# Optimization experiments

Hardware: AMD Instinct MI355X
Metric: run time of the kernel (lower is better)

Reference implementation:

```python
import jax, jax.numpy as jnp
import numpy as np
from jax import lax

B, C_IN, C_OUT, K, STYLE_DIM, H, W = 16, 128, 128, 3, 512, 128, 128
EPS = 1e-8


def setup_inputs() -> dict:
    key = jax.random.key(0)
    k1, k2, k3, k4 = jax.random.split(key, 4)
    x = jax.random.normal(k1, (B, C_IN, H, W), dtype=jnp.float32)
    style_vector = jax.random.normal(k2, (B, STYLE_DIM), dtype=jnp.float32)
    # EqualizedLR(nn.Linear(style_dim, in_channels)): weight ~ N(0,1), bias = 0
    proj_w = jax.random.normal(k3, (C_IN, STYLE_DIM), dtype=jnp.float32)
    proj_b = jnp.zeros((C_IN,), dtype=jnp.float32)
    # base conv weight (1, out, in, k, k) ~ N(0,1)
    weight = jax.random.normal(k4, (1, C_OUT, C_IN, K, K), dtype=jnp.float32)
    return {"x": x, "style_vector": style_vector, "proj_w": proj_w,
            "proj_b": proj_b, "weight": weight}


def reference(x, style_vector, proj_w, proj_b, weight):
    b = x.shape[0]
    # EqualizedLR: scale input by gain / sqrt(fan_in), gain=1, fan_in=style_dim
    scale = 1.0 / jnp.sqrt(jnp.float32(STYLE_DIM))
    style = (style_vector * scale) @ proj_w.T + proj_b          # [b, in]
    # modulate: [1,out,in,k,k] * [b,1,in,1,1] -> [b,out,in,k,k]
    w = weight * style[:, None, :, None, None]
    # demodulate
    demod = lax.rsqrt(jnp.sum(w * w, axis=(2, 3, 4)) + EPS)     # [b, out]
    w = w * demod[:, :, None, None, None]
    # grouped conv with groups=b == per-sample conv; vmap over batch
    pad = K // 2
    def conv_one(xi, wi):
        # xi: [in,H,W], wi: [out,in,k,k]
        return lax.conv_general_dilated(
            xi[None], wi, window_strides=(1, 1),
            padding=[(pad, pad), (pad, pad)],
            dimension_numbers=("NCHW", "OIHW", "NCHW"))[0]
    out = jax.vmap(conv_one)(x, w)                               # [b,out,H,W]
    return out
```

## Files before the change

### kernel.cpp

```cpp
#include <hip/hip_runtime.h>
#include <cstdint>

#define B_   16
#define CIN  128
#define COUT 128
#define SD   512
#define H_   128
#define W_   128

typedef __bf16 bf16x8  __attribute__((ext_vector_type(8)));
typedef float  floatx4 __attribute__((ext_vector_type(4)));
typedef float floatx16 __attribute__((ext_vector_type(16)));

__global__ void style_kernel(const float* __restrict__ sv, const float* __restrict__ pw,
                             const float* __restrict__ pb, float* __restrict__ style) {
    int bid = blockIdx.x;
    int b = bid >> 7, c = bid & 127;
    int lane = threadIdx.x;
    const float* svb = sv + b * SD;
    const float* pwc = pw + (size_t)c * SD;
    float s = 0.f;
#pragma unroll
    for (int i = 0; i < SD; i += 64) s += svb[i + lane] * pwc[i + lane];
#pragma unroll
    for (int off = 32; off > 0; off >>= 1) s += __shfl_down(s, off, 64);
    if (lane == 0) style[b * CIN + c] = s * 0.044194173824159216f + pb[c];
}

__global__ void modw_kernel(const float* __restrict__ weight, const float* __restrict__ style,
                            __bf16* __restrict__ wmod) {
    int bid = blockIdx.x;
    int b = bid >> 7, o = bid & 127;
    int c = threadIdx.x;
    float s = style[b * CIN + c];
    const float* wp = weight + ((size_t)o * CIN + c) * 9;
    float v[9];
    float ss = 0.f;
#pragma unroll
    for (int t = 0; t < 9; ++t) { v[t] = wp[t] * s; ss += v[t] * v[t]; }
#pragma unroll
    for (int off = 32; off > 0; off >>= 1) ss += __shfl_down(ss, off, 64);
    __shared__ float sh[2];
    int wid = c >> 6, lane = c & 63;
    if (lane == 0) sh[wid] = ss;
    __syncthreads();
    float d = rsqrtf(sh[0] + sh[1] + 1e-8f);
    int chunk = c >> 4, ci = c & 15;
#pragma unroll
    for (int t = 0; t < 9; ++t) {
        wmod[(((((size_t)b * 9 + t) * 8 + chunk) * 128 + o) * 16 + ci)] = (__bf16)(v[t] * d);
    }
}

__global__ __launch_bounds__(256)
void xpose_kernel(const float* __restrict__ x, __bf16* __restrict__ xT) {
    __shared__ uint32_t T[4 * 4 * 8 * 32];
    int ch = blockIdx.x;
    int hq = blockIdx.y;
    int b  = blockIdx.z;
    int t  = threadIdx.x;
    int cp = t >> 5;
    int wq = t & 31;
    int c0 = ch * 16 + cp * 2;
    const float* pa = x + (((size_t)b * CIN + c0    ) * H_ + hq * 4) * W_ + wq * 4;
    const float* pc = x + (((size_t)b * CIN + c0 + 1) * H_ + hq * 4) * W_ + wq * 4;
#pragma unroll
    for (int hr = 0; hr < 4; ++hr) {
        floatx4 va = *(const floatx4*)(pa + (size_t)hr * W_);
        floatx4 vb = *(const floatx4*)(pc + (size_t)hr * W_);
#pragma unroll
        for (int j = 0; j < 4; ++j) {
            uint32_t lo = (uint32_t)__builtin_bit_cast(unsigned short, (__bf16)va[j]);
            uint32_t hi = (uint32_t)__builtin_bit_cast(unsigned short, (__bf16)vb[j]);
            T[((hr * 4 + j) * 8 + cp) * 32 + wq] = lo | (hi << 16);
        }
    }
    __syncthreads();
    uint32_t* dst = (uint32_t*)xT + ((((size_t)b * 8 + ch) * H_ + hq * 4) * W_) * 8;
#pragma unroll
    for (int it = 0; it < 8; ++it) {
        int o0 = it * 512 + t * 2;
        int cpr = o0 & 7;
        int w   = (o0 >> 3) & 127;
        int hr  = o0 >> 10;
        int base = ((hr * 4 + (w & 3)) * 8);
        uint32_t v0 = T[(base + cpr    ) * 32 + (w >> 2)];
        uint32_t v1 = T[(base + cpr + 1) * 32 + (w >> 2)];
        uint2 pk; pk.x = v0; pk.y = v1;
        *(uint2*)(dst + o0) = pk;
    }
}

#define WXT 66
__global__ __launch_bounds__(256, 2)
void conv_kernel(const __bf16* __restrict__ xT, const __bf16* __restrict__ wmod,
                 float* __restrict__ out) {
    __shared__ __align__(16) __bf16 Xs[2][4 * WXT * 16];
    int w0 = blockIdx.x * 64;
    int h0 = blockIdx.y * 2;
    int b  = blockIdx.z;
    int tid = threadIdx.x;
    int wv = tid >> 6, lane = tid & 63;
    int n = lane & 31, hf = lane >> 5;
    int obase = (wv & 1) * 64;
    int r = wv >> 1;

    floatx16 acc[2][2];
#pragma unroll
    for (int i = 0; i < 2; ++i)
#pragma unroll
        for (int j = 0; j < 2; ++j)
#pragma unroll
            for (int k = 0; k < 16; ++k) acc[i][j][k] = 0.f;

    const __bf16* xb = xT + (size_t)b * 8 * H_ * W_ * 16;

    bool sact[3], sval[3];
    const __bf16* sptr[3];
    int soff[3];
#pragma unroll
    for (int s = 0; s < 3; ++s) {
        int idx = tid + s * 256;
        bool act = (s < 2) || (tid < 16);
        int row = idx / 132;
        int rem = idx - row * 132;
        int wp = rem >> 1, g = rem & 1;
        int hh = h0 - 1 + row, ww = w0 - 1 + wp;
        sact[s] = act;
        sval[s] = act && (unsigned)hh < (unsigned)H_ && (unsigned)ww < (unsigned)W_;
        sptr[s] = xb + ((size_t)hh * W_ + ww) * 16 + g * 8;
        soff[s] = idx * 8;
    }

    bf16x8 sv[3];
#pragma unroll
    for (int s = 0; s < 3; ++s) {
#pragma unroll
        for (int k = 0; k < 8; ++k) sv[s][k] = (__bf16)0.f;
        if (sval[s]) sv[s] = *(const bf16x8*)(sptr[s]);
    }

    const __bf16* apb = wmod + ((((size_t)b * 9) * 8) * 128 + obase + n) * 16 + hf * 8;

    for (int ch = 0; ch < 8; ++ch) {
        bf16x8 a[9][2];
#pragma unroll
        for (int tap = 0; tap < 9; ++tap) {
            const __bf16* ap = apb + tap * 16384 + ch * 2048;
            a[tap][0] = *(const bf16x8*)ap;
            a[tap][1] = *(const bf16x8*)(ap + 512);
        }
        __bf16* xbuf = Xs[ch & 1];
#pragma unroll
        for (int s = 0; s < 3; ++s)
            if (sact[s]) *(bf16x8*)(xbuf + soff[s]) = sv[s];
        if (ch < 7) {
#pragma unroll
            for (int s = 0; s < 3; ++s) {
#pragma unroll
                for (int k = 0; k < 8; ++k) sv[s][k] = (__bf16)0.f;
                if (sval[s]) sv[s] = *(const bf16x8*)(sptr[s] + (size_t)(ch + 1) * (H_ * W_ * 16));
            }
        }
        __syncthreads();
#pragma unroll
        for (int tap = 0; tap < 9; ++tap) {
            int kh = tap / 3, kw = tap % 3;
            int row = r + kh;
#pragma unroll
            for (int wt = 0; wt < 2; ++wt) {
                int wp = wt * 32 + n + kw;
                bf16x8 bfrag = *(const bf16x8*)(xbuf + (row * WXT + wp) * 16 + hf * 8);
                acc[0][wt] = __builtin_amdgcn_mfma_f32_32x32x16_bf16(a[tap][0], bfrag, acc[0][wt], 0, 0, 0);
                acc[1][wt] = __builtin_amdgcn_mfma_f32_32x32x16_bf16(a[tap][1], bfrag, acc[1][wt], 0, 0, 0);
            }
        }
    }

    float* ob = out + (((size_t)b * COUT) * H_ + (h0 + r)) * W_ + w0;
#pragma unroll
    for (int i = 0; i < 2; ++i) {
#pragma unroll
        for (int reg = 0; reg < 16; ++reg) {
            int o = obase + i * 32 + (reg & 3) + 8 * (reg >> 2) + 4 * hf;
#pragma unroll
            for (int wt = 0; wt < 2; ++wt)
                __builtin_nontemporal_store(acc[i][wt][reg],
                    &ob[(size_t)o * (H_ * W_) + wt * 32 + n]);
        }
    }
}

extern "C" void kernel_launch(void* const* d_in, const int* in_sizes, int n_in,
                              void* d_out, int out_size, void* d_ws, size_t ws_size,
                              hipStream_t stream) {
    const float* x      = (const float*)d_in[0];
    const float* sv     = (const float*)d_in[1];
    const float* pw     = (const float*)d_in[2];
    const float* pb     = (const float*)d_in[3];
    const float* weight = (const float*)d_in[4];
    float* out = (float*)d_out;

    float*  style = (float*)d_ws;
    __bf16* wmod  = (__bf16*)((char*)d_ws + 8192);
    __bf16* xT    = (__bf16*)((char*)d_ws + 8192 + 4718592);

    style_kernel<<<B_ * CIN, 64, 0, stream>>>(sv, pw, pb, style);
    modw_kernel<<<B_ * COUT, 128, 0, stream>>>(weight, style, wmod);
    xpose_kernel<<<dim3(8, 32, B_), 256, 0, stream>>>(x, xT);
    conv_kernel<<<dim3(2, 64, B_), 256, 0, stream>>>(xT, wmod, out);
}
```

Measured before the change: 305.4 us.

## Fuse input transpose into conv kernel with swizzled all-channel LDS tile

Removes the separate transpose kernel and its bf16 workspace round-trip. The conv kernel now reads fp32 NCHW input directly, converts it to bf16 and stages all 128 channels of a 4x66 halo tile into XOR-swizzled shared memory in one pass. The per-channel-chunk double buffering and per-chunk syncs are gone. Each wave now computes all 128 output channels for one row and one half-width, with a 3-deep software-pipelined prefetch of weight fragments across the 72 tap/chunk iterations. In exchange, shared memory grows to about 66KB per block, which may limit occupancy, and the input is staged without overlapping its load with compute.

```diff
diff --git a/kernel.cpp b/kernel.cpp
--- a/kernel.cpp
+++ b/kernel.cpp
@@ -52,141 +52,115 @@
     }
 }
 
-__global__ __launch_bounds__(256)
-void xpose_kernel(const float* __restrict__ x, __bf16* __restrict__ xT) {
-    __shared__ uint32_t T[4 * 4 * 8 * 32];
-    int ch = blockIdx.x;
-    int hq = blockIdx.y;
-    int b  = blockIdx.z;
-    int t  = threadIdx.x;
-    int cp = t >> 5;
-    int wq = t & 31;
-    int c0 = ch * 16 + cp * 2;
-    const float* pa = x + (((size_t)b * CIN + c0    ) * H_ + hq * 4) * W_ + wq * 4;
-    const float* pc = x + (((size_t)b * CIN + c0 + 1) * H_ + hq * 4) * W_ + wq * 4;
-#pragma unroll
-    for (int hr = 0; hr < 4; ++hr) {
-        floatx4 va = *(const floatx4*)(pa + (size_t)hr * W_);
-        floatx4 vb = *(const floatx4*)(pc + (size_t)hr * W_);
-#pragma unroll
-        for (int j = 0; j < 4; ++j) {
-            uint32_t lo = (uint32_t)__builtin_bit_cast(unsigned short, (__bf16)va[j]);
-            uint32_t hi = (uint32_t)__builtin_bit_cast(unsigned short, (__bf16)vb[j]);
-            T[((hr * 4 + j) * 8 + cp) * 32 + wq] = lo | (hi << 16);
-        }
-    }
-    __syncthreads();
-    uint32_t* dst = (uint32_t*)xT + ((((size_t)b * 8 + ch) * H_ + hq * 4) * W_) * 8;
-#pragma unroll
-    for (int it = 0; it < 8; ++it) {
-        int o0 = it * 512 + t * 2;
-        int cpr = o0 & 7;
-        int w   = (o0 >> 3) & 127;
-        int hr  = o0 >> 10;
-        int base = ((hr * 4 + (w & 3)) * 8);
-        uint32_t v0 = T[(base + cpr    ) * 32 + (w >> 2)];
-        uint32_t v1 = T[(base + cpr + 1) * 32 + (w >> 2)];
-        uint2 pk; pk.x = v0; pk.y = v1;
-        *(uint2*)(dst + o0) = pk;
-    }
-}
-
-#define WXT 66
 __global__ __launch_bounds__(256, 2)
-void conv_kernel(const __bf16* __restrict__ xT, const __bf16* __restrict__ wmod,
+void conv_kernel(const float* __restrict__ x, const __bf16* __restrict__ wmod,
                  float* __restrict__ out) {
-    __shared__ __align__(16) __bf16 Xs[2][4 * WXT * 16];
+    __shared__ __align__(16) __bf16 Xs[4 * 66 * 128];
     int w0 = blockIdx.x * 64;
     int h0 = blockIdx.y * 2;
     int b  = blockIdx.z;
     int tid = threadIdx.x;
-    int wv = tid >> 6, lane = tid & 63;
-    int n = lane & 31, hf = lane >> 5;
-    int obase = (wv & 1) * 64;
-    int r = wv >> 1;
 
-    floatx16 acc[2][2];
+    {
+        int p = tid >> 2, row = tid & 3;
+        int hh = h0 - 1 + row;
+        bool rowok = (unsigned)hh < (unsigned)H_;
+        const float* b0 = x + (((size_t)b * CIN + 2 * p) * H_ + (rowok ? hh : 0)) * W_;
+        const float* b1 = b0 + H_ * W_;
+        int ch = p >> 3, g = (p >> 2) & 1, ep = (p & 3) * 2;
+        int robase = row * 66;
+        {
+            float v0 = 0.f, v1 = 0.f;
+            if (rowok && w0 > 0) { v0 = b0[w0 - 1]; v1 = b1[w0 - 1]; }
+            uint32_t pk = (uint32_t)__builtin_bit_cast(unsigned short, (__bf16)v0)
+                        | ((uint32_t)__builtin_bit_cast(unsigned short, (__bf16)v1) << 16);
+            int off = robase * 128 + ((ch ^ 0) * 2 + g) * 8 + ep;
+            *(uint32_t*)(Xs + off) = pk;
+        }
+        {
+            float v0 = 0.f, v1 = 0.f;
+            int w = w0 + 64;
+            if (rowok && w < W_) { v0 = b0[w]; v1 = b1[w]; }
+            uint32_t pk = (uint32_t)__builtin_bit_cast(unsigned short, (__bf16)v0)
+                        | ((uint32_t)__builtin_bit_cast(unsigned short, (__bf16)v1) << 16);
+            int off = (robase + 65) * 128 + ((ch ^ (65 & 7)) * 2 + g) * 8 + ep;
+            *(uint32_t*)(Xs + off) = pk;
+        }
 #pragma unroll
-    for (int i = 0; i < 2; ++i)
+        for (int j = 0; j < 16; ++j) {
+            floatx4 va = {0.f, 0.f, 0.f, 0.f}, vb = {0.f, 0.f, 0.f, 0.f};
+            if (rowok) {
+                va = *(const floatx4*)(b0 + w0 + j * 4);
+                vb = *(const floatx4*)(b1 + w0 + j * 4);
+            }
 #pragma unroll
-        for (int j = 0; j < 2; ++j)
-#pragma unroll
-            for (int k = 0; k < 16; ++k) acc[i][j][k] = 0.f;
-
-    const __bf16* xb = xT + (size_t)b * 8 * H_ * W_ * 16;
-
-    bool sact[3], sval[3];
-    const __bf16* sptr[3];
-    int soff[3];
-#pragma unroll
-    for (int s = 0; s < 3; ++s) {
-        int idx = tid + s * 256;
-        bool act = (s < 2) || (tid < 16);
-        int row = idx / 132;
-        int rem = idx - row * 132;
-        int wp = rem >> 1, g = rem & 1;
-        int hh = h0 - 1 + row, ww = w0 - 1 + wp;
-        sact[s] = act;
-        sval[s] = act && (unsigned)hh < (unsigned)H_ && (unsigned)ww < (unsigned)W_;
-        sptr[s] = xb + ((size_t)hh * W_ + ww) * 16 + g * 8;
-        soff[s] = idx * 8;
-    }
-
-    bf16x8 sv[3];
-#pragma unroll
-    for (int s = 0; s < 3; ++s) {
-#pragma unroll
-        for (int k = 0; k < 8; ++k) sv[s][k] = (__bf16)0.f;
-        if (sval[s]) sv[s] = *(const bf16x8*)(sptr[s]);
-    }
-
-    const __bf16* apb = wmod + ((((size_t)b * 9) * 8) * 128 + obase + n) * 16 + hf * 8;
-
-    for (int ch = 0; ch < 8; ++ch) {
-        bf16x8 a[9][2];
-#pragma unroll
-        for (int tap = 0; tap < 9; ++tap) {
-            const __bf16* ap = apb + tap * 16384 + ch * 2048;
-            a[tap][0] = *(const bf16x8*)ap;
-            a[tap][1] = *(const bf16x8*)(ap + 512);
-        }
-        __bf16* xbuf = Xs[ch & 1];
-#pragma unroll
-        for (int s = 0; s < 3; ++s)
-            if (sact[s]) *(bf16x8*)(xbuf + soff[s]) = sv[s];
-        if (ch < 7) {
-#pragma unroll
-            for (int s = 0; s < 3; ++s) {
-#pragma unroll
-                for (int k = 0; k < 8; ++k) sv[s][k] = (__bf16)0.f;
-                if (sval[s]) sv[s] = *(const bf16x8*)(sptr[s] + (size_t)(ch + 1) * (H_ * W_ * 16));
-            }
-        }
-        __syncthreads();
-#pragma unroll
-        for (int tap = 0; tap < 9; ++tap) {
-            int kh = tap / 3, kw = tap % 3;
-            int row = r + kh;
-#pragma unroll
-            for (int wt = 0; wt < 2; ++wt) {
-                int wp = wt * 32 + n + kw;
-                bf16x8 bfrag = *(const bf16x8*)(xbuf + (row * WXT + wp) * 16 + hf * 8);
-                acc[0][wt] = __builtin_amdgcn_mfma_f32_32x32x16_bf16(a[tap][0], bfrag, acc[0][wt], 0, 0, 0);
-                acc[1][wt] = __builtin_amdgcn_mfma_f32_32x32x16_bf16(a[tap][1], bfrag, acc[1][wt], 0, 0, 0);
+            for (int k = 0; k < 4; ++k) {
+                int wp = j * 4 + 1 + k;
+                uint32_t pk = (uint32_t)__builtin_bit_cast(unsigned short, (__bf16)va[k])
+                            | ((uint32_t)__builtin_bit_cast(unsigned short, (__bf16)vb[k]) << 16);
+                int off = (robase + wp) * 128 + ((ch ^ (wp & 7)) * 2 + g) * 8 + ep;
+                *(uint32_t*)(Xs + off) = pk;
             }
         }
     }
+    __syncthreads();
 
-    float* ob = out + (((size_t)b * COUT) * H_ + (h0 + r)) * W_ + w0;
+    int wv = tid >> 6, lane = tid & 63;
+    int n = lane & 31, hf = lane >> 5;
+    int r = wv & 1, whalf = wv >> 1;
+
+    floatx16 acc[4];
 #pragma unroll
-    for (int i = 0; i < 2; ++i) {
+    for (int i = 0; i < 4; ++i)
+#pragma unroll
+        for (int k = 0; k < 16; ++k) acc[i][k] = 0.f;
+
+    int wb[3], m2[3];
+#pragma unroll
+    for (int kw = 0; kw < 3; ++kw) {
+        int wp = whalf * 32 + n + kw;
+        wb[kw] = wp * 128 + hf * 8;
+        m2[kw] = (wp & 7) * 2;
+    }
+    int roff = r * 8448;
+
+    const __bf16* apb = wmod + (size_t)b * 147456 + n * 16 + hf * 8;
+
+    bf16x8 ab[4][4];
+#define LOADA(slot, it_)                                            \
+    {                                                               \
+        const __bf16* ap = apb + (it_) * 2048;                      \
+        ab[slot][0] = *(const bf16x8*)(ap);                         \
+        ab[slot][1] = *(const bf16x8*)(ap + 512);                   \
+        ab[slot][2] = *(const bf16x8*)(ap + 1024);                  \
+        ab[slot][3] = *(const bf16x8*)(ap + 1536);                  \
+    }
+    LOADA(0, 0) LOADA(1, 1) LOADA(2, 2)
+
+#pragma unroll
+    for (int tap = 0; tap < 9; ++tap) {
+        const int kh = tap / 3, kw = tap % 3;
+#pragma unroll
+        for (int ch = 0; ch < 8; ++ch) {
+            const int it = tap * 8 + ch;
+            const bf16x8 bfrag = *(const bf16x8*)(
+                &Xs[roff + kh * 8448 + wb[kw] + (((2 * ch) ^ m2[kw]) << 3)]);
+            acc[0] = __builtin_amdgcn_mfma_f32_32x32x16_bf16(ab[it & 3][0], bfrag, acc[0], 0, 0, 0);
+            acc[1] = __builtin_amdgcn_mfma_f32_32x32x16_bf16(ab[it & 3][1], bfrag, acc[1], 0, 0, 0);
+            acc[2] = __builtin_amdgcn_mfma_f32_32x32x16_bf16(ab[it & 3][2], bfrag, acc[2], 0, 0, 0);
+            acc[3] = __builtin_amdgcn_mfma_f32_32x32x16_bf16(ab[it & 3][3], bfrag, acc[3], 0, 0, 0);
+            if (it + 3 < 72) LOADA((it + 3) & 3, it + 3)
+        }
+    }
+#undef LOADA
+
+    float* ob = out + (((size_t)b * COUT) * H_ + (h0 + r)) * W_ + w0 + whalf * 32;
+#pragma unroll
+    for (int i = 0; i < 4; ++i) {
 #pragma unroll
         for (int reg = 0; reg < 16; ++reg) {
-            int o = obase + i * 32 + (reg & 3) + 8 * (reg >> 2) + 4 * hf;
-#pragma unroll
-            for (int wt = 0; wt < 2; ++wt)
-                __builtin_nontemporal_store(acc[i][wt][reg],
-                    &ob[(size_t)o * (H_ * W_) + wt * 32 + n]);
+            int o = i * 32 + (reg & 3) + 8 * (reg >> 2) + 4 * hf;
+            __builtin_nontemporal_store(acc[i][reg], &ob[(size_t)o * (H_ * W_) + n]);
         }
     }
 }
@@ -203,10 +177,8 @@
 
     float*  style = (float*)d_ws;
     __bf16* wmod  = (__bf16*)((char*)d_ws + 8192);
-    __bf16* xT    = (__bf16*)((char*)d_ws + 8192 + 4718592);
 
     style_kernel<<<B_ * CIN, 64, 0, stream>>>(sv, pw, pb, style);
     modw_kernel<<<B_ * COUT, 128, 0, stream>>>(weight, style, wmod);
-    xpose_kernel<<<dim3(8, 32, B_), 256, 0, stream>>>(x, xT);
-    conv_kernel<<<dim3(2, 64, B_), 256, 0, stream>>>(xT, wmod, out);
+    conv_kernel<<<dim3(2, 64, B_), 256, 0, stream>>>(x, wmod, out);
 }
```

Measured after the change: 386.1 us. 1.26x slower.
